# Performance work log

Hardware: AMD Instinct MI355X
Metric: run time of the kernel (lower is better)

The kernel has to match this reference:

```python
import jax, jax.numpy as jnp
import numpy as np
import math

B, S, D = 2, 2048, 1024
N_HEAD = 16
EPS = 1e-6

def setup_inputs() -> dict:
    key = jax.random.key(0)
    ks = jax.random.split(key, 12)
    def lin(k):
        kw, kb = jax.random.split(k)
        scale = 1.0 / math.sqrt(D)
        W = jax.random.uniform(kw, (D, D), jnp.float32, -scale, scale)
        b = jax.random.uniform(kb, (D,), jnp.float32, -scale, scale)
        return W, b
    Wq, bq = lin(ks[0]); Wk, bk = lin(ks[1]); Wv, bv = lin(ks[2]); Wo, bo = lin(ks[3])
    return {
        'query': jax.random.normal(ks[4], (B, S, D), jnp.float32),
        'key':   jax.random.normal(ks[5], (B, S, D), jnp.float32),
        'value': jax.random.normal(ks[6], (B, S, D), jnp.float32),
        'mask':  jnp.ones((B, S, S), jnp.int32),
        'Wq': Wq, 'bq': bq, 'Wk': Wk, 'bk': bk, 'Wv': Wv, 'bv': bv,
        'Wo': Wo, 'bo': bo,
        'gamma': jnp.ones((D,), jnp.float32),
        'beta':  jnp.zeros((D,), jnp.float32),
    }

def reference(query, key, value, mask, Wq, bq, Wk, bk, Wv, bv, Wo, bo, gamma, beta):
    b, s, dm = query.shape
    h = N_HEAD
    d = dm // h
    residual = query
    # projections (torch Linear: x @ W.T + b) -> [b, h, s, d]
    def proj(x, W, bias):
        return (x @ W.T + bias).reshape(b, -1, h, d).transpose(0, 2, 1, 3)
    q = proj(query, Wq, bq)
    k = proj(key, Wk, bk)
    v = proj(value, Wv, bv)
    scores = jnp.einsum('bhqd,bhkd->bhqk', q, k) / jnp.sqrt(jnp.float32(d))
    scores = jnp.where(mask[:, None, :, :] == 0, jnp.float32(-1e9), scores)
    p_attn = jax.nn.softmax(scores, axis=-1)  # dropout is identity in eval/reference
    x = jnp.einsum('bhqk,bhkd->bhqd', p_attn, v)
    x = x.transpose(0, 2, 1, 3).reshape(b, -1, h * d)
    x = x @ Wo.T + bo
    x = x + residual
    # LayerNorm with unbiased std and (std + eps) denominator, as in source
    mean = jnp.mean(x, axis=-1, keepdims=True)
    std = jnp.std(x, axis=-1, keepdims=True, ddof=1)
    return gamma * (x - mean) / (std + EPS) + beta
```

## Files before the change

### kernel.cpp

```cpp
#include <hip/hip_runtime.h>
#include <hip/hip_bf16.h>
#include <math.h>
#include <stdint.h>

#define BATCH 2
#define SEQ   2048
#define DMODEL 1024
#define NHEAD 16
#define HDIM  64
#define NROWS (BATCH*SEQ)
#define EPS   1e-6f
#define QSCALE 0.1803368801111204f

typedef float f32x4 __attribute__((ext_vector_type(4)));
typedef short s16x8 __attribute__((ext_vector_type(8)));
typedef unsigned int u32x4 __attribute__((ext_vector_type(4)));

#define OFF_XQ 0
#define OFF_XK 4194304
#define OFF_XV 8388608
#define OFF_WQ 12582912
#define OFF_WK 13631488
#define OFF_WV 14680064
#define OFF_WO 15728640
#define OFF_QB 16777216
#define OFF_KB 20971520
#define OFF_VT 25165824
#define OFF_CM 29360128
#define OFF_MS 29884416

__device__ __forceinline__ unsigned short f2bf(float x) {
    unsigned int u = __builtin_bit_cast(unsigned int, x);
    u += 0x7fff + ((u >> 16) & 1);
    return (unsigned short)(u >> 16);
}

__device__ __forceinline__ void gl_lds16(const void* g, void* l) {
    __builtin_amdgcn_global_load_lds(
        (const __attribute__((address_space(1))) unsigned int*)g,
        (__attribute__((address_space(3))) unsigned int*)(unsigned int)(unsigned long long)l,
        16, 0, 0);
}

__global__ __launch_bounds__(256) void conv_all_kernel(
    const float* __restrict__ q, const float* __restrict__ k, const float* __restrict__ v,
    const float* __restrict__ wq, const float* __restrict__ wk, const float* __restrict__ wv,
    const float* __restrict__ wo, unsigned short* __restrict__ ws)
{
    if (blockIdx.x == 0 && threadIdx.x < 32)
        ((unsigned int*)(ws + OFF_MS))[threadIdx.x] = 0;
    size_t t = ((size_t)blockIdx.x * 256 + threadIdx.x) * 4;
    const float* src; unsigned short* dst; size_t off;
    if (t < 4194304)       { src = q;  dst = ws + OFF_XQ; off = t; }
    else if (t < 8388608)  { src = k;  dst = ws + OFF_XK; off = t - 4194304; }
    else if (t < 12582912) { src = v;  dst = ws + OFF_XV; off = t - 8388608; }
    else if (t < 13631488) { src = wq; dst = ws + OFF_WQ; off = t - 12582912; }
    else if (t < 14680064) { src = wk; dst = ws + OFF_WK; off = t - 13631488; }
    else if (t < 15728640) { src = wv; dst = ws + OFF_WV; off = t - 14680064; }
    else                   { src = wo; dst = ws + OFF_WO; off = t - 15728640; }
    float4 x = *(const float4*)&src[off];
    ushort4 o;
    o.x = f2bf(x.x); o.y = f2bf(x.y); o.z = f2bf(x.z); o.w = f2bf(x.w);
    *(ushort4*)&dst[off] = o;
}

__device__ __forceinline__ void gemm_body(
    const unsigned short* A, const unsigned short* W, int r0, int c0,
    unsigned short* As, unsigned short* Bs, f32x4 acc[4][4])
{
    const int tid  = threadIdx.x;
    const int wave = tid >> 6, lane = tid & 63;
    const int quad = lane >> 4, l15 = lane & 15;
    const int wr = wave >> 1, wc = wave & 1;
    const int aBase0 = (wr*64 + l15)*128 + ((    quad + l15) & 7)*16;
    const int aBase1 = (wr*64 + l15)*128 + ((4 + quad + l15) & 7)*16;
    const int bBase0 = (wc*64 + l15)*128 + ((    quad + l15) & 7)*16;
    const int bBase1 = (wc*64 + l15)*128 + ((4 + quad + l15) & 7)*16;
    for (int k0 = 0; k0 < DMODEL; k0 += 64) {
        __syncthreads();
        #pragma unroll
        for (int r = 0; r < 4; r++) {
            int f   = r * 4096 + tid * 16;
            int row = f >> 7;
            int g   = (((f >> 4) & 7) - row) & 7;
            gl_lds16((const char*)A + (size_t)(r0 + row) * 2048 + k0 * 2 + g * 16,
                     (char*)As + r * 4096 + wave * 1024);
            gl_lds16((const char*)W + (size_t)(c0 + row) * 2048 + k0 * 2 + g * 16,
                     (char*)Bs + r * 4096 + wave * 1024);
        }
        __syncthreads();
        #pragma unroll
        for (int ks = 0; ks < 2; ks++) {
            const int aB = ks ? aBase1 : aBase0;
            const int bB = ks ? bBase1 : bBase0;
            s16x8 a[4], b[4];
            #pragma unroll
            for (int mt = 0; mt < 4; mt++)
                a[mt] = *(const s16x8*)((const char*)As + aB + mt*2048);
            #pragma unroll
            for (int nt = 0; nt < 4; nt++)
                b[nt] = *(const s16x8*)((const char*)Bs + bB + nt*2048);
            #pragma unroll
            for (int mt = 0; mt < 4; mt++)
                #pragma unroll
                for (int nt = 0; nt < 4; nt++)
                    acc[mt][nt] = __builtin_amdgcn_mfma_f32_16x16x32_bf16(a[mt], b[nt], acc[mt][nt], 0, 0, 0);
        }
    }
}

__global__ __launch_bounds__(256) void qkv_gemm_kernel(
    unsigned short* __restrict__ ws,
    const float* __restrict__ bq, const float* __restrict__ bk, const float* __restrict__ bv,
    const int* __restrict__ mask)
{
    const int z = blockIdx.z;
    if (z == 3) {
        unsigned long long* cm = (unsigned long long*)(ws + OFF_CM);
        unsigned int* msum = (unsigned int*)(ws + OFF_MS);
        const int lane = threadIdx.x & 63;
        const int wv = threadIdx.x >> 6;
        const int bid = blockIdx.y * 32 + blockIdx.x;
        const int wbase = (bid * 4 + wv) * 128;
        for (int i = 0; i < 128; i++) {
            int w = wbase + i;
            int s  = w & 2047;
            int kb = (w >> 11) & 31;
            int b  = w >> 16;
            int m = mask[((size_t)b * SEQ + s) * SEQ + kb * 64 + lane];
            unsigned long long bits = __ballot(m != 0);
            if (lane == 0) {
                cm[((size_t)b * 32 + kb) * SEQ + s] = bits;
                if (bits != ~0ull)
                    atomicOr(&msum[(b << 4) | (s >> 7)], 1u << kb);
            }
        }
        return;
    }

    __shared__ __align__(16) unsigned short As[8192];
    __shared__ __align__(16) unsigned short Bs[8192];
    const unsigned short *A, *W;
    int r0, c0;
    if (z != 2) {
        A = ws + (size_t)z * 4194304;
        W = ws + OFF_WQ + (size_t)z * 1048576;
        r0 = blockIdx.x * 128; c0 = blockIdx.y * 128;
    } else {
        A = ws + OFF_WV;
        W = ws + OFF_XV;
        r0 = blockIdx.y * 128; c0 = blockIdx.x * 128;
    }
    const float* bias = (z == 0) ? bq : (z == 1 ? bk : bv);
    unsigned short* outp = ws + OFF_QB + (size_t)z * 4194304;
    const float scale = (z == 0) ? QSCALE : 1.0f;

    f32x4 acc[4][4] = {};
    gemm_body(A, W, r0, c0, As, Bs, acc);

    const int lane = threadIdx.x & 63, wave = threadIdx.x >> 6;
    const int quad = lane >> 4, l15 = lane & 15;
    const int wr = wave >> 1, wc = wave & 1;
    if (z != 2) {
        float bias_v[4];
        #pragma unroll
        for (int nt = 0; nt < 4; nt++) bias_v[nt] = bias[c0 + wc*64 + nt*16 + l15];
        #pragma unroll
        for (int mt = 0; mt < 4; mt++) {
            #pragma unroll
            for (int nt = 0; nt < 4; nt++) {
                int c = c0 + wc*64 + nt*16 + l15;
                int hh = c >> 6, dd = c & 63;
                #pragma unroll
                for (int reg = 0; reg < 4; reg++) {
                    int r = r0 + wr*64 + mt*16 + quad*4 + reg;
                    int bb = r >> 11, ss = r & (SEQ - 1);
                    float val = (acc[mt][nt][reg] + bias_v[nt]) * scale;
                    outp[(((size_t)(bb*NHEAD + hh)) * SEQ + ss) * HDIM + dd] = f2bf(val);
                }
            }
        }
    } else {
        #pragma unroll
        for (int mt = 0; mt < 4; mt++) {
            #pragma unroll
            for (int reg = 0; reg < 4; reg++) {
                int f = r0 + wr*64 + mt*16 + quad*4 + reg;
                int hh = f >> 6, dd = f & 63;
                float bfv = bias[f];
                #pragma unroll
                for (int nt = 0; nt < 4; nt++) {
                    int r = c0 + wc*64 + nt*16 + l15;
                    int bb = r >> 11, ss = r & (SEQ - 1);
                    outp[(((size_t)(bb*NHEAD + hh)) * HDIM + dd) * SEQ + ss] =
                        f2bf(acc[mt][nt][reg] + bfv);
                }
            }
        }
    }
}

__global__ __launch_bounds__(256) void oproj_gemm_kernel(
    const unsigned short* __restrict__ ws, const float* __restrict__ bo,
    const float* __restrict__ resid, float* __restrict__ outf)
{
    __shared__ __align__(16) unsigned short As[8192];
    __shared__ __align__(16) unsigned short Bs[8192];
    const unsigned short* A = ws + OFF_XQ;
    const unsigned short* W = ws + OFF_WO;
    const int r0 = blockIdx.x * 128, c0 = blockIdx.y * 128;

    f32x4 acc[4][4] = {};
    gemm_body(A, W, r0, c0, (unsigned short*)As, (unsigned short*)Bs, acc);

    const int lane = threadIdx.x & 63, wave = threadIdx.x >> 6;
    const int quad = lane >> 4, l15 = lane & 15;
    const int wr = wave >> 1, wc = wave & 1;
    #pragma unroll
    for (int mt = 0; mt < 4; mt++) {
        #pragma unroll
        for (int nt = 0; nt < 4; nt++) {
            int c = c0 + wc*64 + nt*16 + l15;
            float bv = bo[c];
            #pragma unroll
            for (int reg = 0; reg < 4; reg++) {
                int r = r0 + wr*64 + mt*16 + quad*4 + reg;
                size_t idx = (size_t)r * DMODEL + c;
                outf[idx] = acc[mt][nt][reg] + bv + resid[idx];
            }
        }
    }
}

__global__ __launch_bounds__(512) void attn_mfma_kernel(
    const unsigned short* __restrict__ ws,
    const unsigned long long* __restrict__ cmask,
    const unsigned int* __restrict__ msum,
    unsigned short* __restrict__ ab)
{
    const int tid  = threadIdx.x;
    const int wave = tid >> 6, lane = tid & 63;
    const int quad = lane >> 4, l15 = lane & 15;
    const int h = blockIdx.y, b = blockIdx.z;
    const int qw = blockIdx.x * 128 + wave * 16;

    const char* qh = (const char*)(ws + OFF_QB + ((size_t)(b*NHEAD + h)) * SEQ * HDIM);
    const char* kh = (const char*)(ws + OFF_KB + ((size_t)(b*NHEAD + h)) * SEQ * HDIM);
    const char* vh = (const char*)(ws + OFF_VT + ((size_t)(b*NHEAD + h)) * SEQ * HDIM);

    __shared__ __align__(16) char Ks[2][2][8192];
    __shared__ __align__(16) char Vs[2][2][8192];

    const unsigned int chunkflags = msum[(b << 4) | blockIdx.x];

    const int srow = tid >> 3;
    const int sgrp = ((tid & 7) - srow) & 7;
    const int arow = (srow & 0x23) | ((srow & 0x0C) << 1) | ((srow & 0x10) >> 2);

    #define STAGE(bfi, k0)                                                           \
        do {                                                                         \
            gl_lds16(kh + (size_t)((k0) + arow) * 128 + sgrp * 16,                   \
                     Ks[bfi][0] + wave * 1024);                                      \
            gl_lds16(kh + (size_t)((k0) + 64 + arow) * 128 + sgrp * 16,              \
                     Ks[bfi][1] + wave * 1024);                                      \
            gl_lds16(vh + (size_t)srow * 4096 + (size_t)(k0) * 2 + sgrp * 16,        \
                     Vs[bfi][0] + wave * 1024);                                      \
            gl_lds16(vh + (size_t)srow * 4096 + (size_t)((k0) + 64) * 2 + sgrp * 16, \
                     Vs[bfi][1] + wave * 1024);                                      \
        } while (0)

    s16x8 qa[2];
    #pragma unroll
    for (int ks = 0; ks < 2; ks++)
        qa[ks] = *(const s16x8*)(qh + (size_t)(qw + l15) * 128 + ks*64 + quad*16);

    const int fbaseA = l15*128 + ((    quad + l15) & 7) * 16;
    const int fbaseB = l15*128 + ((4 + quad + l15) & 7) * 16;

    s16x8 onesf;
    {
        short so = (short)0x3F80;
        if (l15 == 0) onesf = (s16x8){so, so, so, so, so, so, so, so};
        else          onesf = (s16x8){0, 0, 0, 0, 0, 0, 0, 0};
    }

    f32x4 o[4], lsum = {0.f, 0.f, 0.f, 0.f};
    #pragma unroll
    for (int nt = 0; nt < 4; nt++) o[nt] = (f32x4){0.f, 0.f, 0.f, 0.f};

    STAGE(0, 0);
    int bf = 0;
    for (int k0 = 0; k0 < SEQ; k0 += 128) {
        __syncthreads();
        if (k0 + 128 < SEQ) STAGE(bf ^ 1, k0 + 128);

        #pragma unroll
        for (int half = 0; half < 2; half++) {
            const char* Kb = Ks[bf][half];
            const char* Vb = Vs[bf][half];
            const int kc = (k0 >> 6) + half;
            f32x4 st[4];
            #pragma unroll
            for (int kt = 0; kt < 4; kt++) {
                s16x8 kf0 = *(const s16x8*)(Kb + fbaseA + kt*2048);
                s16x8 kf1 = *(const s16x8*)(Kb + fbaseB + kt*2048);
                f32x4 z = {0.f, 0.f, 0.f, 0.f};
                st[kt] = __builtin_amdgcn_mfma_f32_16x16x32_bf16(kf0, qa[0], z, 0, 0, 0);
                st[kt] = __builtin_amdgcn_mfma_f32_16x16x32_bf16(kf1, qa[1], st[kt], 0, 0, 0);
            }
            if (chunkflags & (1u << kc)) {
                unsigned long long cm =
                    cmask[((size_t)b*32 + kc) * SEQ + qw + l15];
                if (cm != ~0ull) {
                    #pragma unroll
                    for (int kt = 0; kt < 4; kt++)
                        #pragma unroll
                        for (int reg = 0; reg < 4; reg++) {
                            int key = (kt >> 1)*32 + quad*8 + (kt & 1)*4 + reg;
                            if (!((cm >> key) & 1)) st[kt][reg] = -1e9f;
                        }
                }
            }
            #pragma unroll
            for (int ks = 0; ks < 2; ks++) {
                unsigned int pb[8];
                #pragma unroll
                for (int j = 0; j < 8; j++) {
                    int kt = 2*ks + (j >> 2), r = j & 3;
                    pb[j] = __builtin_bit_cast(unsigned int, exp2f(st[kt][r]));
                }
                u32x4 pw;
                pw[0] = __builtin_amdgcn_perm(pb[1], pb[0], 0x07060302u);
                pw[1] = __builtin_amdgcn_perm(pb[3], pb[2], 0x07060302u);
                pw[2] = __builtin_amdgcn_perm(pb[5], pb[4], 0x07060302u);
                pw[3] = __builtin_amdgcn_perm(pb[7], pb[6], 0x07060302u);
                s16x8 pa = __builtin_bit_cast(s16x8, pw);
                lsum = __builtin_amdgcn_mfma_f32_16x16x32_bf16(pa, onesf, lsum, 0, 0, 0);
                const int fb = (ks == 0) ? fbaseA : fbaseB;
                #pragma unroll
                for (int nt = 0; nt < 4; nt++) {
                    s16x8 vf = *(const s16x8*)(Vb + fb + nt*2048);
                    o[nt] = __builtin_amdgcn_mfma_f32_16x16x32_bf16(pa, vf, o[nt], 0, 0, 0);
                }
            }
        }
        bf ^= 1;
    }
    #undef STAGE
    #pragma unroll
    for (int reg = 0; reg < 4; reg++) {
        float lv = __shfl(lsum[reg], lane & 48);
        float inv = 1.f / lv;
        int sg = qw + quad*4 + reg;
        #pragma unroll
        for (int nt = 0; nt < 4; nt++) {
            size_t idx = ((size_t)b * SEQ + sg) * DMODEL + h*HDIM + nt*16 + l15;
            ab[idx] = f2bf(o[nt][reg] * inv);
        }
    }
}

__global__ __launch_bounds__(256) void ln_kernel(
    float* __restrict__ x, const float* __restrict__ gamma,
    const float* __restrict__ beta)
{
    const int row = blockIdx.x;
    const int tid = threadIdx.x;
    float4 vals = *(const float4*)&x[(size_t)row * DMODEL + tid * 4];
    float s  = vals.x + vals.y + vals.z + vals.w;
    float ss = vals.x*vals.x + vals.y*vals.y + vals.z*vals.z + vals.w*vals.w;
    #pragma unroll
    for (int off = 32; off > 0; off >>= 1) {
        s  += __shfl_down(s, off);
        ss += __shfl_down(ss, off);
    }
    __shared__ float sbuf[4], ssbuf[4];
    __shared__ float mean_s, inv_s;
    if ((tid & 63) == 0) { sbuf[tid >> 6] = s; ssbuf[tid >> 6] = ss; }
    __syncthreads();
    if (tid == 0) {
        float S1 = 0.f, S2 = 0.f;
        #pragma unroll
        for (int i = 0; i < 4; i++) { S1 += sbuf[i]; S2 += ssbuf[i]; }
        float mean = S1 * (1.0f / DMODEL);
        float var  = (S2 - (float)DMODEL * mean * mean) * (1.0f / (DMODEL - 1));
        float sd   = sqrtf(fmaxf(var, 0.f));
        mean_s = mean;
        inv_s  = 1.f / (sd + EPS);
    }
    __syncthreads();
    float4 g  = *(const float4*)&gamma[tid * 4];
    float4 bt = *(const float4*)&beta[tid * 4];
    float4 o;
    o.x = g.x * (vals.x - mean_s) * inv_s + bt.x;
    o.y = g.y * (vals.y - mean_s) * inv_s + bt.y;
    o.z = g.z * (vals.z - mean_s) * inv_s + bt.z;
    o.w = g.w * (vals.w - mean_s) * inv_s + bt.w;
    *(float4*)&x[(size_t)row * DMODEL + tid * 4] = o;
}

extern "C" void kernel_launch(void* const* d_in, const int* in_sizes, int n_in,
                              void* d_out, int out_size, void* d_ws, size_t ws_size,
                              hipStream_t stream) {
    const float* query = (const float*)d_in[0];
    const float* key   = (const float*)d_in[1];
    const float* value = (const float*)d_in[2];
    const int*   mask  = (const int*)d_in[3];
    const float* Wq = (const float*)d_in[4];  const float* bq = (const float*)d_in[5];
    const float* Wk = (const float*)d_in[6];  const float* bk = (const float*)d_in[7];
    const float* Wv = (const float*)d_in[8];  const float* bv = (const float*)d_in[9];
    const float* Wo = (const float*)d_in[10]; const float* bo = (const float*)d_in[11];
    const float* gamma = (const float*)d_in[12];
    const float* beta  = (const float*)d_in[13];
    float* out = (float*)d_out;

    unsigned short* ws = (unsigned short*)d_ws;
    unsigned long long* cmask = (unsigned long long*)(ws + OFF_CM);
    unsigned int* msum = (unsigned int*)(ws + OFF_MS);

    conv_all_kernel<<<16384, 256, 0, stream>>>(query, key, value, Wq, Wk, Wv, Wo, ws);
    qkv_gemm_kernel<<<dim3(32, 8, 4), 256, 0, stream>>>(ws, bq, bk, bv, mask);
    attn_mfma_kernel<<<dim3(SEQ/128, NHEAD, BATCH), 512, 0, stream>>>(ws, cmask, msum, ws + OFF_XQ);
    oproj_gemm_kernel<<<dim3(32, 8), 256, 0, stream>>>(ws, bo, query, out);
    ln_kernel<<<NROWS, 256, 0, stream>>>(out, gamma, beta);
}
```

Measured before the change: 320.2 us.

## Double-buffer GEMM LDS tiles and move mask compression to its own kernel

The shared GEMM body now uses two LDS buffers per operand. The global-to-LDS load of the next K tile is issued before the MFMA work on the current tile, and only one barrier is needed per iteration. This is meant to hide global load latency behind compute, at the cost of doubling LDS per block to 64KB, which can lower occupancy. The mask bit-packing, previously done serially by extra z-slice blocks inside the QKV GEMM launch, becomes a separate, more widely parallel kernel, which removes a long-running tail from the GEMM grid.

```diff
diff --git a/kernel.cpp b/kernel.cpp
--- a/kernel.cpp
+++ b/kernel.cpp
@@ -64,9 +64,31 @@
     *(ushort4*)&dst[off] = o;
 }
 
+__global__ __launch_bounds__(256) void mask_compress_kernel(
+    const int* __restrict__ mask, unsigned long long* __restrict__ cm,
+    unsigned int* __restrict__ msum)
+{
+    const int lane = threadIdx.x & 63;
+    const int wid = (blockIdx.x * 256 + threadIdx.x) >> 6;
+    #pragma unroll
+    for (int i = 0; i < 16; i++) {
+        int w = wid + i * 8192;
+        int s  = w & 2047;
+        int kb = (w >> 11) & 31;
+        int b  = w >> 16;
+        int m = mask[((size_t)b * SEQ + s) * SEQ + kb * 64 + lane];
+        unsigned long long bits = __ballot(m != 0);
+        if (lane == 0) {
+            cm[((size_t)b * 32 + kb) * SEQ + s] = bits;
+            if (bits != ~0ull)
+                atomicOr(&msum[(b << 4) | (s >> 7)], 1u << kb);
+        }
+    }
+}
+
 __device__ __forceinline__ void gemm_body(
     const unsigned short* A, const unsigned short* W, int r0, int c0,
-    unsigned short* As, unsigned short* Bs, f32x4 acc[4][4])
+    unsigned short (*As)[8192], unsigned short (*Bs)[8192], f32x4 acc[4][4])
 {
     const int tid  = threadIdx.x;
     const int wave = tid >> 6, lane = tid & 63;
@@ -76,19 +98,26 @@
     const int aBase1 = (wr*64 + l15)*128 + ((4 + quad + l15) & 7)*16;
     const int bBase0 = (wc*64 + l15)*128 + ((    quad + l15) & 7)*16;
     const int bBase1 = (wc*64 + l15)*128 + ((4 + quad + l15) & 7)*16;
+
+    #define GSTAGE(bfi, k0)                                                            \
+        do {                                                                           \
+            _Pragma("unroll")                                                          \
+            for (int r = 0; r < 4; r++) {                                              \
+                int f   = r * 4096 + tid * 16;           \
+                int row = f >> 7;                                 \
+                int g   = (((f >> 4) & 7) - row) & 7;  \
+                gl_lds16((const char*)A + (size_t)(r0 + row) * 2048 + (k0) * 2 + g * 16, \
+                         (char*)As[bfi] + r * 4096 + wave * 1024);                     \
+                gl_lds16((const char*)W + (size_t)(c0 + row) * 2048 + (k0) * 2 + g * 16, \
+                         (char*)Bs[bfi] + r * 4096 + wave * 1024);                     \
+            }                                                                          \
+        } while (0)
+
+    GSTAGE(0, 0);
+    int bf = 0;
     for (int k0 = 0; k0 < DMODEL; k0 += 64) {
         __syncthreads();
-        #pragma unroll
-        for (int r = 0; r < 4; r++) {
-            int f   = r * 4096 + tid * 16;
-            int row = f >> 7;
-            int g   = (((f >> 4) & 7) - row) & 7;
-            gl_lds16((const char*)A + (size_t)(r0 + row) * 2048 + k0 * 2 + g * 16,
-                     (char*)As + r * 4096 + wave * 1024);
-            gl_lds16((const char*)W + (size_t)(c0 + row) * 2048 + k0 * 2 + g * 16,
-                     (char*)Bs + r * 4096 + wave * 1024);
-        }
-        __syncthreads();
+        if (k0 + 64 < DMODEL) GSTAGE(bf ^ 1, k0 + 64);
         #pragma unroll
         for (int ks = 0; ks < 2; ks++) {
             const int aB = ks ? aBase1 : aBase0;
@@ -96,50 +125,28 @@
             s16x8 a[4], b[4];
             #pragma unroll
             for (int mt = 0; mt < 4; mt++)
-                a[mt] = *(const s16x8*)((const char*)As + aB + mt*2048);
+                a[mt] = *(const s16x8*)((const char*)As[bf] + aB + mt*2048);
             #pragma unroll
             for (int nt = 0; nt < 4; nt++)
-                b[nt] = *(const s16x8*)((const char*)Bs + bB + nt*2048);
+                b[nt] = *(const s16x8*)((const char*)Bs[bf] + bB + nt*2048);
             #pragma unroll
             for (int mt = 0; mt < 4; mt++)
                 #pragma unroll
                 for (int nt = 0; nt < 4; nt++)
                     acc[mt][nt] = __builtin_amdgcn_mfma_f32_16x16x32_bf16(a[mt], b[nt], acc[mt][nt], 0, 0, 0);
         }
-    }
+        bf ^= 1;
+    }
+    #undef GSTAGE
 }
 
 __global__ __launch_bounds__(256) void qkv_gemm_kernel(
     unsigned short* __restrict__ ws,
-    const float* __restrict__ bq, const float* __restrict__ bk, const float* __restrict__ bv,
-    const int* __restrict__ mask)
-{
+    const float* __restrict__ bq, const float* __restrict__ bk, const float* __restrict__ bv)
+{
+    __shared__ __align__(16) unsigned short As[2][8192];
+    __shared__ __align__(16) unsigned short Bs[2][8192];
     const int z = blockIdx.z;
-    if (z == 3) {
-        unsigned long long* cm = (unsigned long long*)(ws + OFF_CM);
-        unsigned int* msum = (unsigned int*)(ws + OFF_MS);
-        const int lane = threadIdx.x & 63;
-        const int wv = threadIdx.x >> 6;
-        const int bid = blockIdx.y * 32 + blockIdx.x;
-        const int wbase = (bid * 4 + wv) * 128;
-        for (int i = 0; i < 128; i++) {
-            int w = wbase + i;
-            int s  = w & 2047;
-            int kb = (w >> 11) & 31;
-            int b  = w >> 16;
-            int m = mask[((size_t)b * SEQ + s) * SEQ + kb * 64 + lane];
-            unsigned long long bits = __ballot(m != 0);
-            if (lane == 0) {
-                cm[((size_t)b * 32 + kb) * SEQ + s] = bits;
-                if (bits != ~0ull)
-                    atomicOr(&msum[(b << 4) | (s >> 7)], 1u << kb);
-            }
-        }
-        return;
-    }
-
-    __shared__ __align__(16) unsigned short As[8192];
-    __shared__ __align__(16) unsigned short Bs[8192];
     const unsigned short *A, *W;
     int r0, c0;
     if (z != 2) {
@@ -204,14 +211,14 @@
     const unsigned short* __restrict__ ws, const float* __restrict__ bo,
     const float* __restrict__ resid, float* __restrict__ outf)
 {
-    __shared__ __align__(16) unsigned short As[8192];
-    __shared__ __align__(16) unsigned short Bs[8192];
+    __shared__ __align__(16) unsigned short As[2][8192];
+    __shared__ __align__(16) unsigned short Bs[2][8192];
     const unsigned short* A = ws + OFF_XQ;
     const unsigned short* W = ws + OFF_WO;
     const int r0 = blockIdx.x * 128, c0 = blockIdx.y * 128;
 
     f32x4 acc[4][4] = {};
-    gemm_body(A, W, r0, c0, (unsigned short*)As, (unsigned short*)Bs, acc);
+    gemm_body(A, W, r0, c0, As, Bs, acc);
 
     const int lane = threadIdx.x & 63, wave = threadIdx.x >> 6;
     const int quad = lane >> 4, l15 = lane & 15;
@@ -419,7 +426,8 @@
     unsigned int* msum = (unsigned int*)(ws + OFF_MS);
 
     conv_all_kernel<<<16384, 256, 0, stream>>>(query, key, value, Wq, Wk, Wv, Wo, ws);
-    qkv_gemm_kernel<<<dim3(32, 8, 4), 256, 0, stream>>>(ws, bq, bk, bv, mask);
+    mask_compress_kernel<<<2048, 256, 0, stream>>>(mask, cmask, msum);
+    qkv_gemm_kernel<<<dim3(32, 8, 3), 256, 0, stream>>>(ws, bq, bk, bv);
     attn_mfma_kernel<<<dim3(SEQ/128, NHEAD, BATCH), 512, 0, stream>>>(ws, cmask, msum, ws + OFF_XQ);
     oproj_gemm_kernel<<<dim3(32, 8), 256, 0, stream>>>(ws, bo, query, out);
     ln_kernel<<<NROWS, 256, 0, stream>>>(out, gamma, beta);
```

Measured after the change: 272.5 us. 1.18x faster.
